# Optimization experiments

Hardware: AMD Instinct MI355X
Metric: run time of the kernel (lower is better)

Reference implementation:

```python
import jax, jax.numpy as jnp
import numpy as np


def build_perm(total_channels, num_filters):
    """Replicates Net.permuted_new_perfect's nested slice-copies as one gather index."""
    ncpf = total_channels // num_filters
    tg = num_filters + ncpf * ((num_filters - 1) * num_filters) // 2
    perm = np.zeros(tg * ncpf, dtype=np.int32)
    count = 0
    for i in range(num_filters):
        for j in range(ncpf):
            if j == 0:
                for k in range(i, num_filters):
                    perm[count] = i * ncpf
                    perm[count + 1:count + ncpf] = np.arange(k * ncpf + 1, k * ncpf + ncpf)
                    count += ncpf
            else:
                for k in range(i + 1, num_filters):
                    perm[count + j] = i * ncpf + j
                    perm[count:count + j] = np.arange(k * ncpf, k * ncpf + j)
                    perm[count + j + 1:count + ncpf] = np.arange(k * ncpf + j + 1, k * ncpf + ncpf)
                    count += ncpf
    return jnp.asarray(perm)


PERM1 = build_perm(18, 6)    # 153 gathered channels, 51 groups of 3
PERM2 = build_perm(255, 5)   # 26265 gathered channels, 515 groups of 51


def dw_conv(x, w, b, groups):
    y = jax.lax.conv_general_dilated(
        x, w, window_strides=(1, 1), padding='VALID',
        dimension_numbers=('NCHW', 'OIHW', 'NCHW'),
        feature_group_count=groups)
    return y + b[None, :, None, None]


def maxpool2(x):
    return jax.lax.reduce_window(x, -jnp.inf, jax.lax.max,
                                 (1, 1, 2, 2), (1, 1, 2, 2), 'VALID')


def perm_groupconv(x, perm, w, b):
    # gather channels, then grouped 1x1 conv (each group: ncpf chans -> 1 chan)
    G, ncpf = w.shape
    B, _, H, W = x.shape
    xg = x[:, perm].reshape(B, G, ncpf, H, W)
    return jnp.einsum('bgchw,gc->bghw', xg, w) + b[None, :, None, None]


def setup_inputs() -> dict:
    key = jax.random.key(0)
    ks = jax.random.split(key, 17)
    s = 0.05
    return {
        'x': jax.random.normal(ks[0], (64, 3, 32, 32), jnp.float32),
        'dw1_w': jax.random.normal(ks[1], (18, 1, 5, 5), jnp.float32) * s,
        'dw1_b': jax.random.normal(ks[2], (18,), jnp.float32) * s,
        'pc1_w': jax.random.normal(ks[3], (51, 3), jnp.float32) * s,
        'pc1_b': jax.random.normal(ks[4], (51,), jnp.float32) * s,
        'dw2_w': jax.random.normal(ks[5], (255, 1, 5, 5), jnp.float32) * s,
        'dw2_b': jax.random.normal(ks[6], (255,), jnp.float32) * s,
        'pc2_w': jax.random.normal(ks[7], (515, 51), jnp.float32) * s,
        'pc2_b': jax.random.normal(ks[8], (515,), jnp.float32) * s,
        'oo_w': jax.random.normal(ks[9], (100, 515), jnp.float32) * s,
        'oo_b': jax.random.normal(ks[10], (100,), jnp.float32) * s,
        'fc1_w': jax.random.normal(ks[11], (120, 2500), jnp.float32) * s,
        'fc1_b': jax.random.normal(ks[12], (120,), jnp.float32) * s,
        'fc2_w': jax.random.normal(ks[13], (84, 120), jnp.float32) * s,
        'fc2_b': jax.random.normal(ks[14], (84,), jnp.float32) * s,
        'fc3_w': jax.random.normal(ks[15], (10, 84), jnp.float32) * s,
        'fc3_b': jax.random.normal(ks[16], (10,), jnp.float32) * s,
    }


def reference(x, dw1_w, dw1_b, pc1_w, pc1_b, dw2_w, dw2_b, pc2_w, pc2_b,
              oo_w, oo_b, fc1_w, fc1_b, fc2_w, fc2_b, fc3_w, fc3_b):
    h = dw_conv(x, dw1_w, dw1_b, groups=3)            # [B,18,28,28]
    h = perm_groupconv(h, PERM1, pc1_w, pc1_b)        # [B,51,28,28]
    h = maxpool2(jax.nn.relu(h))                      # [B,51,14,14]
    h = dw_conv(h, dw2_w, dw2_b, groups=51)           # [B,255,10,10]
    h = perm_groupconv(h, PERM2, pc2_w, pc2_b)        # [B,515,10,10]
    h = maxpool2(jax.nn.relu(h))                      # [B,515,5,5]
    h = jax.nn.relu(jnp.einsum('bchw,oc->bohw', h, oo_w) + oo_b[None, :, None, None])  # [B,100,5,5]
    h = h.reshape(h.shape[0], -1)                     # [B,2500]
    h = jax.nn.relu(h @ fc1_w.T + fc1_b)
    h = jax.nn.relu(h @ fc2_w.T + fc2_b)
    return h @ fc3_w.T + fc3_b                        # [B,10]
```

## Files before the change

### kernel.cpp

```cpp
#include <hip/hip_runtime.h>

static constexpr size_t OFF_XT = 0;
static constexpr size_t OFF_H1 = 786432;
static constexpr size_t OFF_H2 = 4399104;
static constexpr size_t OFF_H3 = 6958080;
static constexpr size_t OFF_H4 = 13486080;
static constexpr size_t OFF_H5 = 16782080;
static constexpr size_t OFF_H5B = OFF_H1;
static constexpr size_t OFF_H6 = 17422080;
static constexpr size_t OFF_H7 = 17452800;
static constexpr size_t OFF_M1 = 17474304;
static constexpr size_t OFF_M2 = 17475328;
static constexpr size_t OFF_W2 = 17484032;

struct Meta2 { int g; int special; float wj; int valid; };

__device__ inline void scan_ijk(int F, int ncpf, int g, int& oi, int& oj, int& ok) {
  int cnt = 0;
  for (int i = 0; i < F; ++i)
    for (int j = 0; j < ncpf; ++j) {
      int ks = (j == 0) ? i : i + 1;
      for (int k = ks; k < F; ++k) {
        if (cnt == g) { oi = i; oj = j; ok = k; return; }
        ++cnt;
      }
    }
  oi = 0; oj = 0; ok = 0;
}

__device__ inline float4 f4fma(float4 v, float w, float4 a) {
  a.x = fmaf(v.x, w, a.x); a.y = fmaf(v.y, w, a.y);
  a.z = fmaf(v.z, w, a.z); a.w = fmaf(v.w, w, a.w);
  return a;
}

__global__ void k0_setup(const float* __restrict__ x, const float* __restrict__ pc2_w,
                         float* ws) {
  int bx = blockIdx.x, tid = threadIdx.x;
  if (bx < 96) {
    __shared__ float t[64][33];
    int c = bx >> 5, y = bx & 31;
    for (int r = 0; r < 8; ++r) {
      int b = r * 8 + (tid >> 5), xx = tid & 31;
      t[b][xx] = x[((b * 3 + c) * 32 + y) * 32 + xx];
    }
    __syncthreads();
    float* xT = ws + OFF_XT / 4;
    for (int r = 0; r < 8; ++r) {
      int xx = r * 4 + (tid >> 6), b = tid & 63;
      xT[((c * 32 + y) * 32 + xx) * 64 + b] = t[b][xx];
    }
  } else if (bx == 96) {
    if (tid < 51) {
      int i, j, k; scan_ijk(6, 3, tid, i, j, k);
      int* src1 = (int*)((char*)ws + OFF_M1);
      for (int p = 0; p < 3; ++p)
        src1[tid * 4 + p] = (p == j) ? (i * 3 + j) : (k * 3 + p);
    }
  } else if (bx < 204) {
    int idx = (bx - 97) * 256 + tid;
    if (idx < 536 * 51) {
      int s = idx / 51, p = idx - s * 51;
      int k, base;
      if (s < 8)        { k = 0; base = 0; }
      else if (s < 64)  { k = 1; base = 8; }
      else if (s < 168) { k = 2; base = 64; }
      else if (s < 328) { k = 3; base = 168; }
      else              { k = 4; base = 328; }
      int id2 = s - base;
      int cnt = 51 * k + 1;
      Meta2* m2 = (Meta2*)((char*)ws + OFF_M2);
      float* W2 = (float*)((char*)ws + OFF_W2);
      if (id2 < cnt) {
        int i, j;
        if (id2 <= k) { i = id2; j = 0; }
        else { int t2 = id2 - (k + 1); i = t2 / 50; j = t2 - i * 50 + 1; }
        int off = 205 * i - 51 * ((i * (i - 1)) >> 1);
        int g = (j == 0) ? (off + (k - i))
                         : (off + (5 - i) + (j - 1) * (4 - i) + (k - i - 1));
        W2[s * 51 + p] = (p == j) ? 0.f : pc2_w[g * 51 + p];
        if (p == 0) {
          m2[s].g = g; m2[s].special = i * 51 + j;
          m2[s].wj = pc2_w[g * 51 + j]; m2[s].valid = 1;
        }
      } else {
        W2[s * 51 + p] = 0.f;
        if (p == 0) { m2[s].g = 0; m2[s].special = 0; m2[s].wj = 0.f; m2[s].valid = 0; }
      }
    }
  } else {
    int idx = (bx - 204) * 256 + tid;
    if (idx < 7680) (ws + OFF_H6 / 4)[idx] = 0.f;
  }
}

__global__ void __launch_bounds__(256) k1_dw1(const float* __restrict__ w,
                                              const float* __restrict__ bias, float* ws) {
  const float* xT = ws + OFF_XT / 4;
  float* h1 = ws + OFF_H1 / 4;
  int task = blockIdx.x * 4 + __builtin_amdgcn_readfirstlane(threadIdx.y);
  int l = threadIdx.x;
  int sub = l >> 4, b4 = (l & 15) * 4;
  int o = task / 196, rem = task - o * 196;
  int y = rem / 7, xo = (rem - y * 7) * 4 + sub;
  int c = o / 6;
  float bb = bias[o];
  float4 acc = {bb, bb, bb, bb};
  const float* src = xT + ((c * 32 + y) * 32 + xo) * 64 + b4;
  #pragma unroll
  for (int ky = 0; ky < 5; ++ky)
    #pragma unroll
    for (int kx = 0; kx < 5; ++kx) {
      float4 v = *(const float4*)(src + (ky * 32 + kx) * 64);
      acc = f4fma(v, w[o * 25 + ky * 5 + kx], acc);
    }
  *(float4*)(h1 + ((o * 28 + y) * 28 + xo) * 64 + b4) = acc;
}

__global__ void __launch_bounds__(256) k2_pc1(const float* __restrict__ w,
                                              const float* __restrict__ bias, float* ws) {
  const float* h1 = ws + OFF_H1 / 4;
  const int* src1 = (const int*)((const char*)ws + OFF_M1);
  float* h2 = ws + OFF_H2 / 4;
  int task = blockIdx.x * 4 + __builtin_amdgcn_readfirstlane(threadIdx.y);
  if (task >= 2499) return;
  int l = threadIdx.x;
  int sub = l >> 4, b4 = (l & 15) * 4;
  int g = task / 49, pc = task - g * 49;
  int pp = pc * 4 + sub;
  int py = pp / 14, px = pp - py * 14;
  int s0 = src1[g * 4 + 0], s1 = src1[g * 4 + 1], s2 = src1[g * 4 + 2];
  float w0 = w[g * 3 + 0], w1 = w[g * 3 + 1], w2 = w[g * 3 + 2], bb = bias[g];
  float4 m = {0.f, 0.f, 0.f, 0.f};
  #pragma unroll
  for (int dy = 0; dy < 2; ++dy)
    #pragma unroll
    for (int dx = 0; dx < 2; ++dx) {
      int y = py * 2 + dy, xx = px * 2 + dx;
      float4 a = {bb, bb, bb, bb};
      a = f4fma(*(const float4*)(h1 + ((s0 * 28 + y) * 28 + xx) * 64 + b4), w0, a);
      a = f4fma(*(const float4*)(h1 + ((s1 * 28 + y) * 28 + xx) * 64 + b4), w1, a);
      a = f4fma(*(const float4*)(h1 + ((s2 * 28 + y) * 28 + xx) * 64 + b4), w2, a);
      m.x = fmaxf(m.x, a.x); m.y = fmaxf(m.y, a.y);
      m.z = fmaxf(m.z, a.z); m.w = fmaxf(m.w, a.w);
    }
  *(float4*)(h2 + ((g * 14 + py) * 14 + px) * 64 + b4) = m;
}

__global__ void __launch_bounds__(256) k3_dw2(const float* __restrict__ w,
                                              const float* __restrict__ bias, float* ws) {
  const float* h2 = ws + OFF_H2 / 4;
  float* h3 = ws + OFF_H3 / 4;
  int task = blockIdx.x * 4 + __builtin_amdgcn_readfirstlane(threadIdx.y);
  if (task >= 6375) return;
  int l = threadIdx.x;
  int sub = l >> 4, b4 = (l & 15) * 4;
  int o = task / 25, pc = task - o * 25;
  int p = pc * 4 + sub;
  int y = p / 10, xo = p - y * 10;
  int c = o / 5;
  float bb = bias[o];
  float4 acc = {bb, bb, bb, bb};
  const float* src = h2 + ((c * 14 + y) * 14 + xo) * 64 + b4;
  #pragma unroll
  for (int ky = 0; ky < 5; ++ky)
    #pragma unroll
    for (int kx = 0; kx < 5; ++kx) {
      float4 v = *(const float4*)(src + (ky * 14 + kx) * 64);
      acc = f4fma(v, w[o * 25 + ky * 5 + kx], acc);
    }
  int py = y >> 1, dy = y & 1, px = xo >> 1, dx = xo & 1;
  *(float4*)(h3 + ((o * 25 + py * 5 + px) * 4 + dy * 2 + dx) * 64 + b4) = acc;
}

__global__ void __launch_bounds__(256) k4_pc2(const float* __restrict__ bias, float* ws) {
  const float* h3 = ws + OFF_H3 / 4;
  const float* W2 = (const float*)((const char*)ws + OFF_W2);
  const Meta2* m2 = (const Meta2*)((const char*)ws + OFF_M2);
  float* h4 = ws + OFF_H4 / 4;
  int b = threadIdx.x;
  int wv = __builtin_amdgcn_readfirstlane(threadIdx.y);
  int pyx = blockIdx.x;
  int chunk = blockIdx.y;
  int k;
  if (chunk < 1) k = 0; else if (chunk < 8) k = 1; else if (chunk < 21) k = 2;
  else if (chunk < 41) k = 3; else k = 4;
  int s0 = chunk * 8 + wv * 2;
  float acc[2][4];
  #pragma unroll
  for (int m = 0; m < 2; ++m)
    #pragma unroll
    for (int q = 0; q < 4; ++q) acc[m][q] = 0.f;
  const float* hb = h3 + (size_t)(k * 51 * 100 + pyx * 4) * 64 + b;
  const float* wr0 = W2 + (s0 + 0) * 51;
  const float* wr1 = W2 + (s0 + 1) * 51;
  for (int p = 0; p < 51; ++p) {
    float v0 = hb[p * 6400 + 0];
    float v1 = hb[p * 6400 + 64];
    float v2 = hb[p * 6400 + 128];
    float v3 = hb[p * 6400 + 192];
    float wa = wr0[p], wb = wr1[p];
    acc[0][0] = fmaf(v0, wa, acc[0][0]);
    acc[0][1] = fmaf(v1, wa, acc[0][1]);
    acc[0][2] = fmaf(v2, wa, acc[0][2]);
    acc[0][3] = fmaf(v3, wa, acc[0][3]);
    acc[1][0] = fmaf(v0, wb, acc[1][0]);
    acc[1][1] = fmaf(v1, wb, acc[1][1]);
    acc[1][2] = fmaf(v2, wb, acc[1][2]);
    acc[1][3] = fmaf(v3, wb, acc[1][3]);
  }
  #pragma unroll
  for (int m = 0; m < 2; ++m) {
    Meta2 mm = m2[s0 + m];
    if (!mm.valid) continue;
    const float* hs = h3 + (size_t)(mm.special * 100 + pyx * 4) * 64 + b;
    float bb = bias[mm.g];
    float r0 = fmaf(hs[0],   mm.wj, acc[m][0]) + bb;
    float r1 = fmaf(hs[64],  mm.wj, acc[m][1]) + bb;
    float r2 = fmaf(hs[128], mm.wj, acc[m][2]) + bb;
    float r3 = fmaf(hs[192], mm.wj, acc[m][3]) + bb;
    float r = fmaxf(fmaxf(r0, r1), fmaxf(r2, r3));
    h4[(mm.g * 25 + pyx) * 64 + b] = fmaxf(r, 0.f);
  }
}

__global__ void __launch_bounds__(256) k5_oo(const float* __restrict__ w, float* ws) {
  const float* h4 = ws + OFF_H4 / 4;
  __shared__ float red[4][4][64];
  int lane = threadIdx.x;
  int wv = __builtin_amdgcn_readfirstlane(threadIdx.y);
  int pyx = blockIdx.x, og = blockIdx.y, ks = blockIdx.z;
  int kb = ks ? 258 : 0;
  int kn = ks ? 257 : 258;
  int q = kn >> 2, r = kn & 3;
  int base = __builtin_amdgcn_readfirstlane(kb + wv * q + (wv < r ? wv : r));
  int n = q + (wv < r ? 1 : 0);
  const float* w0 = w + (og * 4 + 0) * 515;
  const float* w1 = w + (og * 4 + 1) * 515;
  const float* w2 = w + (og * 4 + 2) * 515;
  const float* w3 = w + (og * 4 + 3) * 515;
  const float* hp = h4 + pyx * 64 + lane;
  float a0 = 0.f, a1 = 0.f, a2 = 0.f, a3 = 0.f;
  #pragma unroll 4
  for (int i = 0; i < n; ++i) {
    int c = base + i;
    float v = hp[c * 1600];
    a0 = fmaf(v, w0[c], a0);
    a1 = fmaf(v, w1[c], a1);
    a2 = fmaf(v, w2[c], a2);
    a3 = fmaf(v, w3[c], a3);
  }
  red[wv][0][lane] = a0; red[wv][1][lane] = a1;
  red[wv][2][lane] = a2; red[wv][3][lane] = a3;
  __syncthreads();
  if (wv == 0) {
    float* h5p = ws + (ks ? OFF_H5B : OFF_H5) / 4;
    #pragma unroll
    for (int m = 0; m < 4; ++m) {
      float s = red[0][m][lane] + red[1][m][lane] + red[2][m][lane] + red[3][m][lane];
      h5p[((og * 4 + m) * 25 + pyx) * 64 + lane] = s;
    }
  }
}

__global__ void __launch_bounds__(256) k6_fc1(const float* __restrict__ w,
                                              const float* __restrict__ oo_b, float* ws) {
  const float* h5a = ws + OFF_H5 / 4;
  const float* h5b = ws + OFF_H5B / 4;
  float* h6 = ws + OFF_H6 / 4;
  __shared__ float red[4][4][64];
  int lane = threadIdx.x;
  int wv = __builtin_amdgcn_readfirstlane(threadIdx.y);
  int og = blockIdx.x, ks = blockIdx.y;
  int kb = ks * 156 + (ks < 4 ? ks : 4);
  int kn = 156 + (ks < 4 ? 1 : 0);
  int q = kn >> 2, r = kn & 3;
  int base = __builtin_amdgcn_readfirstlane(kb + wv * q + (wv < r ? wv : r));
  int n = q + (wv < r ? 1 : 0);
  const float* w0 = w + (og * 4 + 0) * 2500;
  const float* w1 = w + (og * 4 + 1) * 2500;
  const float* w2 = w + (og * 4 + 2) * 2500;
  const float* w3 = w + (og * 4 + 3) * 2500;
  float a0 = 0.f, a1 = 0.f, a2 = 0.f, a3 = 0.f;
  #pragma unroll 4
  for (int i = 0; i < n; ++i) {
    int k = base + i;
    float v = fmaxf(h5a[k * 64 + lane] + h5b[k * 64 + lane] + oo_b[k / 25], 0.f);
    a0 = fmaf(v, w0[k], a0);
    a1 = fmaf(v, w1[k], a1);
    a2 = fmaf(v, w2[k], a2);
    a3 = fmaf(v, w3[k], a3);
  }
  red[wv][0][lane] = a0; red[wv][1][lane] = a1;
  red[wv][2][lane] = a2; red[wv][3][lane] = a3;
  __syncthreads();
  if (wv == 0) {
    #pragma unroll
    for (int m = 0; m < 4; ++m) {
      float s = red[0][m][lane] + red[1][m][lane] + red[2][m][lane] + red[3][m][lane];
      atomicAdd(&h6[(og * 4 + m) * 64 + lane], s);
    }
  }
}

__global__ void __launch_bounds__(256) k7_fc2(const float* __restrict__ w,
                                              const float* __restrict__ fc1_b,
                                              const float* __restrict__ bias, float* ws) {
  const float* h6 = ws + OFF_H6 / 4;
  float* h7 = ws + OFF_H7 / 4;
  __shared__ float red[4][64];
  int lane = threadIdx.x & 63, wv = threadIdx.x >> 6;
  int o = blockIdx.x;
  float acc = 0.f;
  int i0 = wv * 30;
  #pragma unroll 5
  for (int i = i0; i < i0 + 30; ++i) {
    float v = fmaxf(h6[i * 64 + lane] + fc1_b[i], 0.f);
    acc = fmaf(v, w[o * 120 + i], acc);
  }
  red[wv][lane] = acc;
  __syncthreads();
  if (threadIdx.x < 64) {
    float s = red[0][lane] + red[1][lane] + red[2][lane] + red[3][lane] + bias[o];
    h7[o * 64 + lane] = fmaxf(s, 0.f);
  }
}

__global__ void __launch_bounds__(256) k8_fc3(const float* __restrict__ w,
                                              const float* __restrict__ bias,
                                              float* out, const float* ws) {
  const float* h7 = ws + OFF_H7 / 4;
  __shared__ float red[4][64];
  int lane = threadIdx.x & 63, wv = threadIdx.x >> 6;
  int o = blockIdx.x;
  float acc = 0.f;
  int i0 = wv * 21;
  #pragma unroll 7
  for (int i = i0; i < i0 + 21; ++i)
    acc = fmaf(h7[i * 64 + lane], w[o * 84 + i], acc);
  red[wv][lane] = acc;
  __syncthreads();
  if (threadIdx.x < 64) {
    float s = red[0][lane] + red[1][lane] + red[2][lane] + red[3][lane] + bias[o];
    out[lane * 10 + o] = s;
  }
}

extern "C" void kernel_launch(void* const* d_in, const int* in_sizes, int n_in,
                              void* d_out, int out_size, void* d_ws, size_t ws_size,
                              hipStream_t stream) {
  const float* x     = (const float*)d_in[0];
  const float* dw1_w = (const float*)d_in[1];
  const float* dw1_b = (const float*)d_in[2];
  const float* pc1_w = (const float*)d_in[3];
  const float* pc1_b = (const float*)d_in[4];
  const float* dw2_w = (const float*)d_in[5];
  const float* dw2_b = (const float*)d_in[6];
  const float* pc2_w = (const float*)d_in[7];
  const float* pc2_b = (const float*)d_in[8];
  const float* oo_w  = (const float*)d_in[9];
  const float* oo_b  = (const float*)d_in[10];
  const float* fc1_w = (const float*)d_in[11];
  const float* fc1_b = (const float*)d_in[12];
  const float* fc2_w = (const float*)d_in[13];
  const float* fc2_b = (const float*)d_in[14];
  const float* fc3_w = (const float*)d_in[15];
  const float* fc3_b = (const float*)d_in[16];
  float* ws = (float*)d_ws;
  float* out = (float*)d_out;

  hipLaunchKernelGGL(k0_setup, dim3(234), dim3(256), 0, stream, x, pc2_w, ws);
  hipLaunchKernelGGL(k1_dw1, dim3(882), dim3(64, 4), 0, stream, dw1_w, dw1_b, ws);
  hipLaunchKernelGGL(k2_pc1, dim3(625), dim3(64, 4), 0, stream, pc1_w, pc1_b, ws);
  hipLaunchKernelGGL(k3_dw2, dim3(1594), dim3(64, 4), 0, stream, dw2_w, dw2_b, ws);
  hipLaunchKernelGGL(k4_pc2, dim3(25, 67), dim3(64, 4), 0, stream, pc2_b, ws);
  hipLaunchKernelGGL(k5_oo, dim3(25, 25, 2), dim3(64, 4), 0, stream, oo_w, ws);
  hipLaunchKernelGGL(k6_fc1, dim3(30, 16), dim3(64, 4), 0, stream, fc1_w, oo_b, ws);
  hipLaunchKernelGGL(k7_fc2, dim3(84), dim3(256), 0, stream, fc2_w, fc1_b, fc2_b, ws);
  hipLaunchKernelGGL(k8_fc3, dim3(10), dim3(256), 0, stream, fc3_w, fc3_b, out, ws);
}
```

Baseline: 150.2 us.

## Widen pc2 register tiling, split fc1 further, fuse fc2/fc3 into one block

The pc2 grouped conv now uses a transposed weight layout and a task-based grid in which each wave computes up to 16 output groups per spatial position. Each h3 load is reused across 16 accumulators instead of 2, which cuts redundant activation reads. fc1 doubles its K-split to 32 slices to expose more blocks, and fc2 and fc3 are merged into a single one-block kernel that stages activations in LDS, saving a launch. In exchange, the 64-float accumulator array raises register pressure and lowers occupancy for pc2, and the single-block tail runs serially on one CU.

```diff
diff --git a/kernel.cpp b/kernel.cpp
--- a/kernel.cpp
+++ b/kernel.cpp
@@ -14,6 +14,14 @@
 static constexpr size_t OFF_W2 = 17484032;
 
 struct Meta2 { int g; int special; float wj; int valid; };
+
+__device__ const int g_s0tab[35] = {
+  0,
+  8, 24, 40, 56,
+  64, 80, 96, 112, 128, 144, 160,
+  168, 184, 200, 216, 232, 248, 264, 280, 296, 312,
+  328, 344, 360, 376, 392, 408, 424, 440, 456, 472, 488, 504, 520
+};
 
 __device__ inline void scan_ijk(int F, int ncpf, int g, int& oi, int& oj, int& ok) {
   int cnt = 0;
@@ -70,7 +78,7 @@
       int id2 = s - base;
       int cnt = 51 * k + 1;
       Meta2* m2 = (Meta2*)((char*)ws + OFF_M2);
-      float* W2 = (float*)((char*)ws + OFF_W2);
+      float* W2T = (float*)((char*)ws + OFF_W2);
       if (id2 < cnt) {
         int i, j;
         if (id2 <= k) { i = id2; j = 0; }
@@ -78,13 +86,13 @@
         int off = 205 * i - 51 * ((i * (i - 1)) >> 1);
         int g = (j == 0) ? (off + (k - i))
                          : (off + (5 - i) + (j - 1) * (4 - i) + (k - i - 1));
-        W2[s * 51 + p] = (p == j) ? 0.f : pc2_w[g * 51 + p];
+        W2T[p * 536 + s] = (p == j) ? 0.f : pc2_w[g * 51 + p];
         if (p == 0) {
           m2[s].g = g; m2[s].special = i * 51 + j;
           m2[s].wj = pc2_w[g * 51 + j]; m2[s].valid = 1;
         }
       } else {
-        W2[s * 51 + p] = 0.f;
+        W2T[p * 536 + s] = 0.f;
         if (p == 0) { m2[s].g = 0; m2[s].special = 0; m2[s].wj = 0.f; m2[s].valid = 0; }
       }
     }
@@ -173,54 +181,61 @@
   *(float4*)(h3 + ((o * 25 + py * 5 + px) * 4 + dy * 2 + dx) * 64 + b4) = acc;
 }
 
-__global__ void __launch_bounds__(256) k4_pc2(const float* __restrict__ bias, float* ws) {
+__global__ void k4_pc2(const float* __restrict__ bias, float* ws) {
   const float* h3 = ws + OFF_H3 / 4;
-  const float* W2 = (const float*)((const char*)ws + OFF_W2);
+  const float* W2T = (const float*)((const char*)ws + OFF_W2);
   const Meta2* m2 = (const Meta2*)((const char*)ws + OFF_M2);
   float* h4 = ws + OFF_H4 / 4;
-  int b = threadIdx.x;
+  int lane = threadIdx.x;
   int wv = __builtin_amdgcn_readfirstlane(threadIdx.y);
-  int pyx = blockIdx.x;
-  int chunk = blockIdx.y;
-  int k;
-  if (chunk < 1) k = 0; else if (chunk < 8) k = 1; else if (chunk < 21) k = 2;
-  else if (chunk < 41) k = 3; else k = 4;
-  int s0 = chunk * 8 + wv * 2;
-  float acc[2][4];
+  int task = blockIdx.x * 4 + wv;
+  if (task >= 875) return;
+  int pyx = task / 35, g = task - pyx * 35;
+  int s0 = g_s0tab[g];
+  int k, cend;
+  if (s0 < 8)        { k = 0; cend = 8; }
+  else if (s0 < 64)  { k = 1; cend = 64; }
+  else if (s0 < 168) { k = 2; cend = 168; }
+  else if (s0 < 328) { k = 3; cend = 328; }
+  else               { k = 4; cend = 536; }
+  int n = cend - s0; if (n > 16) n = 16;
+
+  float acc[16][4];
   #pragma unroll
-  for (int m = 0; m < 2; ++m)
+  for (int m = 0; m < 16; ++m)
     #pragma unroll
     for (int q = 0; q < 4; ++q) acc[m][q] = 0.f;
-  const float* hb = h3 + (size_t)(k * 51 * 100 + pyx * 4) * 64 + b;
-  const float* wr0 = W2 + (s0 + 0) * 51;
-  const float* wr1 = W2 + (s0 + 1) * 51;
+
+  const float* hb = h3 + (size_t)(k * 5100 + pyx * 4) * 64 + lane;
+  const float* wb = W2T + s0;
   for (int p = 0; p < 51; ++p) {
     float v0 = hb[p * 6400 + 0];
     float v1 = hb[p * 6400 + 64];
     float v2 = hb[p * 6400 + 128];
     float v3 = hb[p * 6400 + 192];
-    float wa = wr0[p], wb = wr1[p];
-    acc[0][0] = fmaf(v0, wa, acc[0][0]);
-    acc[0][1] = fmaf(v1, wa, acc[0][1]);
-    acc[0][2] = fmaf(v2, wa, acc[0][2]);
-    acc[0][3] = fmaf(v3, wa, acc[0][3]);
-    acc[1][0] = fmaf(v0, wb, acc[1][0]);
-    acc[1][1] = fmaf(v1, wb, acc[1][1]);
-    acc[1][2] = fmaf(v2, wb, acc[1][2]);
-    acc[1][3] = fmaf(v3, wb, acc[1][3]);
-  }
-  #pragma unroll
-  for (int m = 0; m < 2; ++m) {
+    const float* wr = wb + p * 536;
+    #pragma unroll
+    for (int m = 0; m < 16; ++m) {
+      float w = wr[m];
+      acc[m][0] = fmaf(v0, w, acc[m][0]);
+      acc[m][1] = fmaf(v1, w, acc[m][1]);
+      acc[m][2] = fmaf(v2, w, acc[m][2]);
+      acc[m][3] = fmaf(v3, w, acc[m][3]);
+    }
+  }
+
+  for (int m = 0; m < 16; ++m) {
+    if (m >= n) break;
     Meta2 mm = m2[s0 + m];
     if (!mm.valid) continue;
-    const float* hs = h3 + (size_t)(mm.special * 100 + pyx * 4) * 64 + b;
+    const float* hs = h3 + (size_t)(mm.special * 100 + pyx * 4) * 64 + lane;
     float bb = bias[mm.g];
     float r0 = fmaf(hs[0],   mm.wj, acc[m][0]) + bb;
     float r1 = fmaf(hs[64],  mm.wj, acc[m][1]) + bb;
     float r2 = fmaf(hs[128], mm.wj, acc[m][2]) + bb;
     float r3 = fmaf(hs[192], mm.wj, acc[m][3]) + bb;
     float r = fmaxf(fmaxf(r0, r1), fmaxf(r2, r3));
-    h4[(mm.g * 25 + pyx) * 64 + b] = fmaxf(r, 0.f);
+    h4[(mm.g * 25 + pyx) * 64 + lane] = fmaxf(r, 0.f);
   }
 }
 
@@ -272,8 +287,8 @@
   int lane = threadIdx.x;
   int wv = __builtin_amdgcn_readfirstlane(threadIdx.y);
   int og = blockIdx.x, ks = blockIdx.y;
-  int kb = ks * 156 + (ks < 4 ? ks : 4);
-  int kn = 156 + (ks < 4 ? 1 : 0);
+  int kb = ks * 78 + (ks < 4 ? ks : 4);
+  int kn = 78 + (ks < 4 ? 1 : 0);
   int q = kn >> 2, r = kn & 3;
   int base = __builtin_amdgcn_readfirstlane(kb + wv * q + (wv < r ? wv : r));
   int n = q + (wv < r ? 1 : 0);
@@ -303,46 +318,39 @@
   }
 }
 
-__global__ void __launch_bounds__(256) k7_fc2(const float* __restrict__ w,
-                                              const float* __restrict__ fc1_b,
-                                              const float* __restrict__ bias, float* ws) {
+__global__ void __launch_bounds__(256) k78_tail(const float* __restrict__ fc1_b,
+                                                const float* __restrict__ fc2_w,
+                                                const float* __restrict__ fc2_b,
+                                                const float* __restrict__ fc3_w,
+                                                const float* __restrict__ fc3_b,
+                                                float* out, const float* ws) {
+  __shared__ float h6l[120 * 64];
+  __shared__ float h7l[84 * 64];
   const float* h6 = ws + OFF_H6 / 4;
-  float* h7 = ws + OFF_H7 / 4;
-  __shared__ float red[4][64];
-  int lane = threadIdx.x & 63, wv = threadIdx.x >> 6;
-  int o = blockIdx.x;
-  float acc = 0.f;
-  int i0 = wv * 30;
-  #pragma unroll 5
-  for (int i = i0; i < i0 + 30; ++i) {
-    float v = fmaxf(h6[i * 64 + lane] + fc1_b[i], 0.f);
-    acc = fmaf(v, w[o * 120 + i], acc);
-  }
-  red[wv][lane] = acc;
+  int tid = threadIdx.x;
+  int lane = tid & 63;
+  int wv = __builtin_amdgcn_readfirstlane(tid >> 6);
+
+  for (int i = tid; i < 7680; i += 256)
+    h6l[i] = fmaxf(h6[i] + fc1_b[i >> 6], 0.f);
   __syncthreads();
-  if (threadIdx.x < 64) {
-    float s = red[0][lane] + red[1][lane] + red[2][lane] + red[3][lane] + bias[o];
-    h7[o * 64 + lane] = fmaxf(s, 0.f);
-  }
-}
-
-__global__ void __launch_bounds__(256) k8_fc3(const float* __restrict__ w,
-                                              const float* __restrict__ bias,
-                                              float* out, const float* ws) {
-  const float* h7 = ws + OFF_H7 / 4;
-  __shared__ float red[4][64];
-  int lane = threadIdx.x & 63, wv = threadIdx.x >> 6;
-  int o = blockIdx.x;
-  float acc = 0.f;
-  int i0 = wv * 21;
-  #pragma unroll 7
-  for (int i = i0; i < i0 + 21; ++i)
-    acc = fmaf(h7[i * 64 + lane], w[o * 84 + i], acc);
-  red[wv][lane] = acc;
+
+  for (int j = 0; j < 21; ++j) {
+    int o = wv * 21 + j;
+    float acc = fc2_b[o];
+    #pragma unroll 8
+    for (int i = 0; i < 120; ++i)
+      acc = fmaf(h6l[i * 64 + lane], fc2_w[o * 120 + i], acc);
+    h7l[o * 64 + lane] = fmaxf(acc, 0.f);
+  }
   __syncthreads();
-  if (threadIdx.x < 64) {
-    float s = red[0][lane] + red[1][lane] + red[2][lane] + red[3][lane] + bias[o];
-    out[lane * 10 + o] = s;
+
+  for (int o = wv; o < 10; o += 4) {
+    float acc = fc3_b[o];
+    #pragma unroll 7
+    for (int i = 0; i < 84; ++i)
+      acc = fmaf(h7l[i * 64 + lane], fc3_w[o * 84 + i], acc);
+    out[lane * 10 + o] = acc;
   }
 }
 
@@ -373,9 +381,9 @@
   hipLaunchKernelGGL(k1_dw1, dim3(882), dim3(64, 4), 0, stream, dw1_w, dw1_b, ws);
   hipLaunchKernelGGL(k2_pc1, dim3(625), dim3(64, 4), 0, stream, pc1_w, pc1_b, ws);
   hipLaunchKernelGGL(k3_dw2, dim3(1594), dim3(64, 4), 0, stream, dw2_w, dw2_b, ws);
-  hipLaunchKernelGGL(k4_pc2, dim3(25, 67), dim3(64, 4), 0, stream, pc2_b, ws);
+  hipLaunchKernelGGL(k4_pc2, dim3(219), dim3(64, 4), 0, stream, pc2_b, ws);
   hipLaunchKernelGGL(k5_oo, dim3(25, 25, 2), dim3(64, 4), 0, stream, oo_w, ws);
-  hipLaunchKernelGGL(k6_fc1, dim3(30, 16), dim3(64, 4), 0, stream, fc1_w, oo_b, ws);
-  hipLaunchKernelGGL(k7_fc2, dim3(84), dim3(256), 0, stream, fc2_w, fc1_b, fc2_b, ws);
-  hipLaunchKernelGGL(k8_fc3, dim3(10), dim3(256), 0, stream, fc3_w, fc3_b, out, ws);
-}
+  hipLaunchKernelGGL(k6_fc1, dim3(30, 32), dim3(64, 4), 0, stream, fc1_w, oo_b, ws);
+  hipLaunchKernelGGL(k78_tail, dim3(1), dim3(256), 0, stream,
+                     fc1_b, fc2_w, fc2_b, fc3_w, fc3_b, out, ws);
+}
```

Result: slower. 232.0 us (+54.5%).
